# Optimization experiments

Measured on AMD Instinct MI355X. Metric: run time of the kernel, lower is better.

The kernel has to match this reference:

```python
import jax, jax.numpy as jnp
from jax import lax
import numpy as np

C = 384   # d_model (channels)
DI = 768  # d_inner = expand * C
S = 256   # d_state = min(C, 256)
R = 24    # dt_rank = ceil(C / 16)
K = 4     # d_conv
B = 2
L = 512


def setup_inputs():
    key = jax.random.key(0)
    ks = jax.random.split(key, 12)
    n = jax.random.normal
    return {
        'x': n(ks[0], (B, L, C), jnp.float32),
        'ln1_g': jnp.ones((C,), jnp.float32),
        'ln1_b': jnp.zeros((C,), jnp.float32),
        'ln2_g': jnp.ones((C,), jnp.float32),
        'ln2_b': jnp.zeros((C,), jnp.float32),
        'head_w': n(ks[1], (C, C), jnp.float32) * C ** -0.5,
        'head_b': jnp.zeros((C,), jnp.float32),
        'in_proj_w': n(ks[2], (2 * DI, C), jnp.float32) * C ** -0.5,
        'conv_w': n(ks[3], (DI, 1, K), jnp.float32) * 0.3,
        'conv_b': n(ks[4], (DI,), jnp.float32) * 0.05,
        'x_proj_w': n(ks[5], (R + 2 * S, DI), jnp.float32) * DI ** -0.5,
        'dt_proj_w': n(ks[6], (DI, R), jnp.float32) * R ** -0.5,
        'dt_proj_b': jnp.log(jnp.expm1(jax.random.uniform(ks[7], (DI,), jnp.float32, 1e-3, 0.1))),
        'A_log': jnp.log(jnp.broadcast_to(jnp.arange(1, S + 1, dtype=jnp.float32), (DI, S))),
        'D': jnp.ones((DI,), jnp.float32),
        'out_proj_w': n(ks[8], (C, DI), jnp.float32) * DI ** -0.5,
    }


def _layernorm(x, g, b, eps=1e-5):
    mu = jnp.mean(x, -1, keepdims=True)
    var = jnp.var(x, -1, keepdims=True)  # biased, as torch LayerNorm
    return (x - mu) * lax.rsqrt(var + eps) * g + b


def _mamba(u, in_proj_w, conv_w, conv_b, x_proj_w, dt_proj_w, dt_proj_b, A_log, D, out_proj_w):
    bsz = u.shape[0]
    xz = u @ in_proj_w.T                                  # (B,L,2*DI)
    x_in, z = jnp.split(xz, 2, axis=-1)
    # causal depthwise conv1d along L (left-pad K-1)
    xc = lax.conv_general_dilated(x_in.transpose(0, 2, 1), conv_w, (1,), [(K - 1, 0)],
                                  feature_group_count=DI)  # (B,DI,L)
    x_act = jax.nn.silu(xc.transpose(0, 2, 1) + conv_b)    # (B,L,DI)
    x_dbl = x_act @ x_proj_w.T                             # (B,L,R+2S)
    dt, Bm, Cm = jnp.split(x_dbl, [R, R + S], axis=-1)
    dt = jax.nn.softplus(dt @ dt_proj_w.T + dt_proj_b)     # (B,L,DI)
    A = -jnp.exp(A_log)                                    # (DI,S)
    dtu = dt * x_act                                       # (B,L,DI)

    def body(h, inp):
        dt_t, dtu_t, B_t, C_t = inp                        # (B,DI),(B,DI),(B,S),(B,S)
        dA = jnp.exp(dt_t[:, :, None] * A)                 # (B,DI,S) discretized A
        h = dA * h + dtu_t[:, :, None] * B_t[:, None, :]
        y = jnp.einsum('bds,bs->bd', h, C_t)
        return h, y

    h0 = jnp.zeros((bsz, DI, S), u.dtype)
    xs = (dt.transpose(1, 0, 2), dtu.transpose(1, 0, 2),
          Bm.transpose(1, 0, 2), Cm.transpose(1, 0, 2))
    _, ys = lax.scan(jax.checkpoint(body), h0, xs)         # ys: (L,B,DI)
    y = ys.transpose(1, 0, 2) + D * x_act                  # + D * u skip
    y = y * jax.nn.silu(z)                                 # gated output
    return y @ out_proj_w.T                                # (B,L,C)


def reference(x, ln1_g, ln1_b, ln2_g, ln2_b, head_w, head_b, in_proj_w, conv_w, conv_b,
              x_proj_w, dt_proj_w, dt_proj_b, A_log, D, out_proj_w):
    x = _mamba(_layernorm(x, ln1_g, ln1_b), in_proj_w, conv_w, conv_b, x_proj_w,
               dt_proj_w, dt_proj_b, A_log, D, out_proj_w) + x
    x = _layernorm(x, ln2_g, ln2_b) @ head_w.T + head_b + x
    return x
```

## Files before the change

### kernel.cpp

```cpp
#include <hip/hip_runtime.h>
#include <hip/hip_bf16.h>

#define Cc   384
#define DI   768
#define Ss   256
#define Rr   24
#define Kk   4
#define Bb   2
#define Ll   512
#define NROWS (Bb*Ll)
#define XZW  (2*DI)
#define XDBLW (Rr+2*Ss)
#define TC   128
#define NCH  (Ll/TC)
#define NDP  (DI/2)

#define NWA (XZW*Cc)
#define NWB (XDBLW*DI)
#define NWC (Cc*DI)
#define NWD (Cc*Cc)
#define NWTOT (NWA+NWB+NWC+NWD)
#define NWCVT_BLK (NWTOT/4/256)
#define PREP_GRID (NWCVT_BLK + NROWS/2)

typedef short v8s __attribute__((ext_vector_type(8)));
typedef float v4f __attribute__((ext_vector_type(4)));
typedef float v2f __attribute__((ext_vector_type(2)));

#if __has_builtin(__builtin_amdgcn_exp2f)
#define EXP2(x) __builtin_amdgcn_exp2f(x)
#else
#define EXP2(x) __expf((x) * 0.69314718056f)
#endif
#define L2E 1.44269504089f
#define LN2 0.69314718056f

__device__ __forceinline__ unsigned short f2bf(float f) {
    unsigned int u = __float_as_uint(f);
    unsigned int r = (u + 0x7fffu + ((u >> 16) & 1u)) >> 16;
    return (unsigned short)r;
}
__device__ __forceinline__ float bf2f(unsigned int hi) {
    return __uint_as_float(hi << 16);
}

__global__ __launch_bounds__(256) void prep_kernel(
    const float* __restrict__ wa, unsigned short* __restrict__ oa,
    const float* __restrict__ wb, unsigned short* __restrict__ ob,
    const float* __restrict__ wc, unsigned short* __restrict__ oc,
    const float* __restrict__ wd, unsigned short* __restrict__ od,
    const float* __restrict__ x, const float* __restrict__ g,
    const float* __restrict__ bia, unsigned short* __restrict__ uout)
{
    __shared__ float sm[2][4];
    if (blockIdx.x < NWCVT_BLK) {
        int i = (blockIdx.x * 256 + threadIdx.x) * 4;
        const float* src; unsigned short* dst;
        if (i < NWA)                   { src = wa + i;                     dst = oa + i; }
        else if (i < NWA + NWB)        { src = wb + (i - NWA);             dst = ob + (i - NWA); }
        else if (i < NWA + NWB + NWC)  { src = wc + (i - NWA - NWB);       dst = oc + (i - NWA - NWB); }
        else if (i < NWTOT)            { src = wd + (i - NWA - NWB - NWC); dst = od + (i - NWA - NWB - NWC); }
        else return;
        float4 v = *(const float4*)src;
        dst[0] = f2bf(v.x); dst[1] = f2bf(v.y); dst[2] = f2bf(v.z); dst[3] = f2bf(v.w);
        return;
    }
    const int half = threadIdx.x >> 7;
    const int tid  = threadIdx.x & 127;
    const int row  = (blockIdx.x - NWCVT_BLK) * 2 + half;
    const float* xr = x + (size_t)row * Cc;
    float v[3];
    float s = 0.f, q = 0.f;
#pragma unroll
    for (int i = 0; i < 3; ++i) {
        v[i] = xr[tid + i * 128];
        s += v[i];
        q += v[i] * v[i];
    }
#pragma unroll
    for (int m = 32; m; m >>= 1) {
        s += __shfl_xor(s, m);
        q += __shfl_xor(q, m);
    }
    if ((tid & 63) == 0) {
        sm[half][tid >> 6] = s;
        sm[half][2 + (tid >> 6)] = q;
    }
    __syncthreads();
    const float S_ = sm[half][0] + sm[half][1];
    const float Q_ = sm[half][2] + sm[half][3];
    const float mu = S_ * (1.f / Cc);
    const float var = Q_ * (1.f / Cc) - mu * mu;
    const float r = rsqrtf(var + 1e-5f);
#pragma unroll
    for (int i = 0; i < 3; ++i) {
        const int c = tid + i * 128;
        uout[(size_t)row * Cc + c] = f2bf((v[i] - mu) * r * g[c] + bia[c]);
    }
}

__global__ __launch_bounds__(128) void ln_bf_kernel(
    const float* __restrict__ x, const float* __restrict__ g,
    const float* __restrict__ b, unsigned short* __restrict__ out)
{
    const int row = blockIdx.x;
    const float* xr = x + (size_t)row * Cc;
    float v[3];
    float s = 0.f, q = 0.f;
#pragma unroll
    for (int i = 0; i < 3; ++i) {
        v[i] = xr[threadIdx.x + i * 128];
        s += v[i];
        q += v[i] * v[i];
    }
#pragma unroll
    for (int m = 32; m; m >>= 1) {
        s += __shfl_xor(s, m);
        q += __shfl_xor(q, m);
    }
    __shared__ float sm[4];
    if ((threadIdx.x & 63) == 0) {
        sm[threadIdx.x >> 6] = s;
        sm[2 + (threadIdx.x >> 6)] = q;
    }
    __syncthreads();
    const float S_ = sm[0] + sm[1];
    const float Q_ = sm[2] + sm[3];
    const float mu = S_ * (1.f / Cc);
    const float var = Q_ * (1.f / Cc) - mu * mu;
    const float r = rsqrtf(var + 1e-5f);
#pragma unroll
    for (int i = 0; i < 3; ++i) {
        const int c = threadIdx.x + i * 128;
        out[(size_t)row * Cc + c] = f2bf((v[i] - mu) * r * g[c] + b[c]);
    }
}

template<int EPI>
__global__ __launch_bounds__(256) void gemm_mfma(
    const unsigned short* __restrict__ A, const unsigned short* __restrict__ W,
    const float* __restrict__ bias, const float* __restrict__ res,
    float* __restrict__ out, int M, int N, int Kd)
{
    const int wave = threadIdx.x >> 6;
    const int lane = threadIdx.x & 63;
    const int m0 = blockIdx.y * 64 + (wave >> 1) * 32;
    const int n0 = blockIdx.x * 64 + (wave & 1) * 32;
    const int lr = lane & 15;
    const int quad = lane >> 4;

    v4f acc00 = {0.f,0.f,0.f,0.f}, acc01 = {0.f,0.f,0.f,0.f};
    v4f acc10 = {0.f,0.f,0.f,0.f}, acc11 = {0.f,0.f,0.f,0.f};

    int nA = n0 + lr;      if (nA >= N) nA = N - 1;
    int nB = n0 + 16 + lr; if (nB >= N) nB = N - 1;
    const unsigned short* Ar0 = A + (size_t)(m0 + lr) * Kd + quad * 8;
    const unsigned short* Ar1 = A + (size_t)(m0 + 16 + lr) * Kd + quad * 8;
    const unsigned short* Wr0 = W + (size_t)nA * Kd + quad * 8;
    const unsigned short* Wr1 = W + (size_t)nB * Kd + quad * 8;

    v8s a0 = *(const v8s*)(Ar0);
    v8s a1 = *(const v8s*)(Ar1);
    v8s b0 = *(const v8s*)(Wr0);
    v8s b1 = *(const v8s*)(Wr1);

    for (int k0 = 32; k0 < Kd; k0 += 32) {
        const v8s na0 = *(const v8s*)(Ar0 + k0);
        const v8s na1 = *(const v8s*)(Ar1 + k0);
        const v8s nb0 = *(const v8s*)(Wr0 + k0);
        const v8s nb1 = *(const v8s*)(Wr1 + k0);
        acc00 = __builtin_amdgcn_mfma_f32_16x16x32_bf16(a0, b0, acc00, 0, 0, 0);
        acc01 = __builtin_amdgcn_mfma_f32_16x16x32_bf16(a0, b1, acc01, 0, 0, 0);
        acc10 = __builtin_amdgcn_mfma_f32_16x16x32_bf16(a1, b0, acc10, 0, 0, 0);
        acc11 = __builtin_amdgcn_mfma_f32_16x16x32_bf16(a1, b1, acc11, 0, 0, 0);
        a0 = na0; a1 = na1; b0 = nb0; b1 = nb1;
    }
    acc00 = __builtin_amdgcn_mfma_f32_16x16x32_bf16(a0, b0, acc00, 0, 0, 0);
    acc01 = __builtin_amdgcn_mfma_f32_16x16x32_bf16(a0, b1, acc01, 0, 0, 0);
    acc10 = __builtin_amdgcn_mfma_f32_16x16x32_bf16(a1, b0, acc10, 0, 0, 0);
    acc11 = __builtin_amdgcn_mfma_f32_16x16x32_bf16(a1, b1, acc11, 0, 0, 0);

    v4f accs[2][2] = {{acc00, acc01}, {acc10, acc11}};
#pragma unroll
    for (int i = 0; i < 2; ++i) {
#pragma unroll
        for (int j = 0; j < 2; ++j) {
#pragma unroll
            for (int r = 0; r < 4; ++r) {
                const int row = m0 + i * 16 + quad * 4 + r;
                const int col = n0 + j * 16 + lr;
                if (col < N) {
                    float v = accs[i][j][r];
                    if (EPI >= 2) v += bias[col];
                    if (EPI >= 1) v += res[(size_t)row * N + col];
                    out[(size_t)row * N + col] = v;
                }
            }
        }
    }
}

__global__ __launch_bounds__(256) void conv_kernel(
    const float* __restrict__ xz, const float* __restrict__ cw,
    const float* __restrict__ cb, float* __restrict__ xact,
    unsigned short* __restrict__ xact_bf)
{
    const int d = blockIdx.x * 256 + threadIdx.x;
    const int l0 = blockIdx.y * 8;
    const int b  = blockIdx.z;
    const float4 w = *(const float4*)&cw[d * 4];
    const float bias = cb[d];
    float xv[11];
#pragma unroll
    for (int k = 0; k < 11; ++k) {
        const int l = l0 - 3 + k;
        xv[k] = (l >= 0 && l < Ll) ? xz[(size_t)(b * Ll + l) * XZW + d] : 0.f;
    }
#pragma unroll
    for (int i = 0; i < 8; ++i) {
        float acc = bias + w.x * xv[i] + w.y * xv[i + 1] + w.z * xv[i + 2] + w.w * xv[i + 3];
        const float sv = acc / (1.f + __expf(-acc));
        const size_t row = (size_t)(b * Ll + l0 + i);
        xact[row * DI + d] = sv;
        xact_bf[row * DI + d] = f2bf(sv);
    }
}

__global__ __launch_bounds__(NDP) void dtpack_kernel(
    const float* __restrict__ xdbl, const float* __restrict__ w,
    const float* __restrict__ bias, const float* __restrict__ xact,
    const float* __restrict__ xz, const float* __restrict__ Dp,
    float4* __restrict__ pkA, float2* __restrict__ pkB, float4* __restrict__ epk)
{
    const int dp = threadIdx.x;
    const int row0 = blockIdx.x * 4;
    __shared__ float r[4][Rr];
    if (threadIdx.x < 4 * Rr) {
        const int rr = threadIdx.x / Rr, ii = threadIdx.x % Rr;
        r[rr][ii] = xdbl[(size_t)(row0 + rr) * XDBLW + ii];
    }
    __syncthreads();
    const int d0 = dp * 2;
    float w0r[Rr], w1r[Rr];
    const float* wp = w + (size_t)d0 * Rr;
#pragma unroll
    for (int i = 0; i < Rr; ++i) { w0r[i] = wp[i]; w1r[i] = wp[Rr + i]; }
    const float b0 = bias[d0], b1 = bias[d0 + 1];
    const float D0 = Dp[d0], D1 = Dp[d0 + 1];
#pragma unroll
    for (int rr = 0; rr < 4; ++rr) {
        const int row = row0 + rr;
        float a0 = b0, a1 = b1;
#pragma unroll
        for (int i = 0; i < Rr; ++i) {
            a0 = fmaf(r[rr][i], w0r[i], a0);
            a1 = fmaf(r[rr][i], w1r[i], a1);
        }
        const float aL0 = a0 * L2E, aL1 = a1 * L2E;
        const float dtL0 = (a0 > 20.f) ? aL0 : __log2f(1.f + EXP2(aL0));
        const float dtL1 = (a1 > 20.f) ? aL1 : __log2f(1.f + EXP2(aL1));
        const float dt0 = dtL0 * LN2;
        const float dt1 = dtL1 * LN2;
        const float2 xa = *(const float2*)&xact[(size_t)row * DI + d0];
        const float2 z  = *(const float2*)&xz[(size_t)row * XZW + DI + d0];
        const float sz0 = z.x / (1.f + __expf(-z.x));
        const float sz1 = z.y / (1.f + __expf(-z.y));
        const size_t idx = (size_t)dp * NROWS + row;
        pkA[idx] = make_float4(dtL0, dt0 * xa.x, dtL1, dt1 * xa.y);
        pkB[idx] = make_float2(EXP2(-dtL0), EXP2(-dtL1));
        epk[idx] = make_float4(D0 * xa.x, sz0, D1 * xa.y, sz1);
    }
}

__global__ __launch_bounds__(64) void scan_pass1(
    const float4* __restrict__ pkA, const float2* __restrict__ pkB,
    const float* __restrict__ xdbl,
    unsigned short* __restrict__ hws, float* __restrict__ dtsum)
{
    const int lane = threadIdx.x;
    const int dp = blockIdx.x;
    const int d0 = dp * 2;
    const int c  = blockIdx.y;
    const int b  = blockIdx.z;
    const int s0 = lane * 4;
    const float s1f = (float)(s0 + 1);

    v2f h[4] = {{0.f,0.f},{0.f,0.f},{0.f,0.f},{0.f,0.f}};
    float ds0 = 0.f, ds1 = 0.f;

    const int row0 = b * Ll + c * TC;
    const size_t pk0 = (size_t)dp * NROWS + row0;
#pragma unroll 4
    for (int t = 0; t < TC; ++t) {
        const float4 P  = pkA[pk0 + t];
        const float2 Wv = pkB[pk0 + t];
        const float4 Bv = *(const float4*)&xdbl[(size_t)(row0 + t) * XDBLW + Rr + s0];
        ds0 += P.x; ds1 += P.z;
        v2f e = { EXP2(-P.x * s1f), EXP2(-P.z * s1f) };
        const v2f wv = { Wv.x, Wv.y };
        const v2f dtu = { P.y, P.w };
        h[0] = e * h[0] + dtu * Bv.x;  e *= wv;
        h[1] = e * h[1] + dtu * Bv.y;  e *= wv;
        h[2] = e * h[2] + dtu * Bv.z;  e *= wv;
        h[3] = e * h[3] + dtu * Bv.w;
    }
    const size_t base0 = (((size_t)(b * DI + d0) * NCH) + c) * Ss + s0;
    const size_t base1 = base0 + (size_t)NCH * Ss;
    uint2 o0, o1;
    o0.x = (unsigned int)f2bf(h[0].x) | ((unsigned int)f2bf(h[1].x) << 16);
    o0.y = (unsigned int)f2bf(h[2].x) | ((unsigned int)f2bf(h[3].x) << 16);
    o1.x = (unsigned int)f2bf(h[0].y) | ((unsigned int)f2bf(h[1].y) << 16);
    o1.y = (unsigned int)f2bf(h[2].y) | ((unsigned int)f2bf(h[3].y) << 16);
    *(uint2*)&hws[base0] = o0;
    *(uint2*)&hws[base1] = o1;
    if ((lane & 31) == 0) {
        const int dd = d0 + (lane >> 5);
        dtsum[(size_t)(b * DI + dd) * NCH + c] = (lane == 0) ? ds0 : ds1;
    }
}

__global__ __launch_bounds__(64) void scan_pass23(
    const float4* __restrict__ pkA, const float2* __restrict__ pkB,
    const float4* __restrict__ epk, const float* __restrict__ xdbl,
    const unsigned short* __restrict__ hws, const float* __restrict__ dtsum,
    unsigned short* __restrict__ yg_bf)
{
    __shared__ float pbuf[32][66];
    const int lane = threadIdx.x;
    const int dp = blockIdx.x;
    const int d0 = dp * 2;
    const int c  = blockIdx.y;
    const int b  = blockIdx.z;
    const int s0 = lane * 4;
    const float s1f = (float)(s0 + 1);

    const size_t base0 = (((size_t)(b * DI + d0) * NCH) + c) * Ss + s0;
    const size_t base1 = base0 + (size_t)NCH * Ss;

    v2f h[4] = {{0.f,0.f},{0.f,0.f},{0.f,0.f},{0.f,0.f}};
    {
        const float* dsr0 = dtsum + (size_t)(b * DI + d0) * NCH;
        const float* dsr1 = dsr0 + NCH;
        float Dl0 = 0.f, Dl1 = 0.f;
        for (int cp = c - 1; cp >= 0; --cp) {
            const size_t off = (size_t)(c - cp) * Ss;
            const uint2 hu0 = *(const uint2*)&hws[base0 - off];
            const uint2 hu1 = *(const uint2*)&hws[base1 - off];
            v2f e = { EXP2(-Dl0 * s1f), EXP2(-Dl1 * s1f) };
            const v2f wv = { EXP2(-Dl0), EXP2(-Dl1) };
            const v2f hl0 = { bf2f(hu0.x & 0xffffu), bf2f(hu1.x & 0xffffu) };
            const v2f hl1 = { bf2f(hu0.x >> 16),     bf2f(hu1.x >> 16) };
            const v2f hl2 = { bf2f(hu0.y & 0xffffu), bf2f(hu1.y & 0xffffu) };
            const v2f hl3 = { bf2f(hu0.y >> 16),     bf2f(hu1.y >> 16) };
            h[0] += e * hl0;  e *= wv;
            h[1] += e * hl1;  e *= wv;
            h[2] += e * hl2;  e *= wv;
            h[3] += e * hl3;
            Dl0 += dsr0[cp]; Dl1 += dsr1[cp];
        }
    }

    const int row0 = b * Ll + c * TC;
    const size_t pk0 = (size_t)dp * NROWS + row0;
    const int pidx = (lane >> 5) * 33 + (lane & 31);
    for (int seg = 0; seg < TC / 32; ++seg) {
        const int tb = seg * 32;
#pragma unroll 4
        for (int tl = 0; tl < 32; ++tl) {
            const int t = tb + tl;
            const float4 P  = pkA[pk0 + t];
            const float2 Wv = pkB[pk0 + t];
            const float4 Bv = *(const float4*)&xdbl[(size_t)(row0 + t) * XDBLW + Rr + s0];
            const float4 Cv = *(const float4*)&xdbl[(size_t)(row0 + t) * XDBLW + Rr + Ss + s0];
            v2f e = { EXP2(-P.x * s1f), EXP2(-P.z * s1f) };
            const v2f wv = { Wv.x, Wv.y };
            const v2f dtu = { P.y, P.w };
            h[0] = e * h[0] + dtu * Bv.x;  e *= wv;
            h[1] = e * h[1] + dtu * Bv.y;  e *= wv;
            h[2] = e * h[2] + dtu * Bv.z;  e *= wv;
            h[3] = e * h[3] + dtu * Bv.w;

            v2f p = h[0] * Cv.x + h[1] * Cv.y;
            p += h[2] * Cv.z + h[3] * Cv.w;
            float p0 = p.x, p1 = p.y;
            p0 += __shfl_xor(p0, 32);
            p1 += __shfl_xor(p1, 32);
            pbuf[tl][pidx] = (lane < 32) ? p0 : p1;
        }
        __syncthreads();
        {
            const int tl = lane >> 1;
            const int ch = lane & 1;
            const float* pr = &pbuf[tl][ch * 33];
            float sum = 0.f;
#pragma unroll
            for (int j = 0; j < 32; ++j) sum += pr[j];
            const float4 ev = epk[pk0 + tb + tl];
            const float Dxa = ch ? ev.z : ev.x;
            const float sz  = ch ? ev.w : ev.y;
            yg_bf[(size_t)(row0 + tb + tl) * DI + d0 + ch] = f2bf((sum + Dxa) * sz);
        }
        __syncthreads();
    }
}

extern "C" void kernel_launch(void* const* d_in, const int* in_sizes, int n_in,
                              void* d_out, int out_size, void* d_ws, size_t ws_size,
                              hipStream_t stream)
{
    const float* x         = (const float*)d_in[0];
    const float* ln1_g     = (const float*)d_in[1];
    const float* ln1_b     = (const float*)d_in[2];
    const float* ln2_g     = (const float*)d_in[3];
    const float* ln2_b     = (const float*)d_in[4];
    const float* head_w    = (const float*)d_in[5];
    const float* head_b    = (const float*)d_in[6];
    const float* in_proj_w = (const float*)d_in[7];
    const float* conv_w    = (const float*)d_in[8];
    const float* conv_b    = (const float*)d_in[9];
    const float* x_proj_w  = (const float*)d_in[10];
    const float* dt_proj_w = (const float*)d_in[11];
    const float* dt_proj_b = (const float*)d_in[12];
    const float* Dvec      = (const float*)d_in[14];
    const float* out_proj_w= (const float*)d_in[15];
    float* out = (float*)d_out;

    float* ws    = (float*)d_ws;
    float4* pkA  = (float4*)ws;
    float4* epk  = pkA + (size_t)NDP * NROWS;
    float2* pkB  = (float2*)(epk + (size_t)NDP * NROWS);
    float* xz    = (float*)(pkB + (size_t)NDP * NROWS);
    float* xact  = xz    + (size_t)NROWS * XZW;
    float* xdbl  = xact  + (size_t)NROWS * DI;
    float* x1    = xdbl  + (size_t)NROWS * XDBLW;
    float* dtsum = x1    + (size_t)NROWS * Cc;
    unsigned short* hws     = (unsigned short*)(dtsum + (size_t)Bb * DI * NCH);
    unsigned short* u_bf    = hws     + (size_t)Bb * DI * NCH * Ss;
    unsigned short* xact_bf = u_bf    + (size_t)NROWS * Cc;
    unsigned short* yg_bf   = xact_bf + (size_t)NROWS * DI;
    unsigned short* t2_bf   = yg_bf   + (size_t)NROWS * DI;
    unsigned short* ipw_bf  = t2_bf   + (size_t)NROWS * Cc;
    unsigned short* xpw_bf  = ipw_bf  + (size_t)XZW * Cc;
    unsigned short* opw_bf  = xpw_bf  + (size_t)XDBLW * DI;
    unsigned short* hw_bf   = opw_bf  + (size_t)Cc * DI;

    prep_kernel<<<PREP_GRID, 256, 0, stream>>>(
        in_proj_w, ipw_bf, x_proj_w, xpw_bf, out_proj_w, opw_bf, head_w, hw_bf,
        x, ln1_g, ln1_b, u_bf);
    gemm_mfma<0><<<dim3(24, 16), 256, 0, stream>>>(u_bf, ipw_bf, nullptr, nullptr,
                                                   xz, NROWS, XZW, Cc);
    conv_kernel<<<dim3(3, Ll / 8, Bb), 256, 0, stream>>>(xz, conv_w, conv_b,
                                                         xact, xact_bf);
    gemm_mfma<0><<<dim3(9, 16), 256, 0, stream>>>(xact_bf, xpw_bf, nullptr, nullptr,
                                                  xdbl, NROWS, XDBLW, DI);
    dtpack_kernel<<<NROWS / 4, NDP, 0, stream>>>(xdbl, dt_proj_w, dt_proj_b,
                                                 xact, xz, Dvec, pkA, pkB, epk);
    scan_pass1<<<dim3(NDP, NCH, Bb), 64, 0, stream>>>(pkA, pkB, xdbl, hws, dtsum);
    scan_pass23<<<dim3(NDP, NCH, Bb), 64, 0, stream>>>(pkA, pkB, epk, xdbl, hws,
                                                       dtsum, yg_bf);
    gemm_mfma<1><<<dim3(6, 16), 256, 0, stream>>>(yg_bf, opw_bf, nullptr, x,
                                                  x1, NROWS, Cc, DI);
    ln_bf_kernel<<<NROWS, 128, 0, stream>>>(x1, ln2_g, ln2_b, t2_bf);
    gemm_mfma<2><<<dim3(6, 16), 256, 0, stream>>>(t2_bf, hw_bf, head_b, x1,
                                                  out, NROWS, Cc, Cc);
}
```

Measured before the change: 216.1 us.

## Fold first-chunk output into scan pass one and trim redundant chunk work

Chunk 0 of the chunked selective scan needs no carried-in state, so the first scan kernel now computes its gated outputs directly, using a shared-memory reduction over the state dimension. The second kernel then only handles chunks 1..NCH-1. The first kernel also skips the last chunk, whose end state is never consumed. This removes roughly one chunk of work from each scan kernel, at the cost of load imbalance: chunk-0 blocks in the first kernel do extra C-loads, reductions and syncs.

Result: no change. 212.9 us (-1.5%).

```diff
diff --git a/kernel.cpp b/kernel.cpp
--- a/kernel.cpp
+++ b/kernel.cpp
@@ -272,11 +272,13 @@
     }
 }
 
-__global__ __launch_bounds__(64) void scan_pass1(
+__global__ __launch_bounds__(64) void scan_a(
     const float4* __restrict__ pkA, const float2* __restrict__ pkB,
-    const float* __restrict__ xdbl,
-    unsigned short* __restrict__ hws, float* __restrict__ dtsum)
-{
+    const float4* __restrict__ epk, const float* __restrict__ xdbl,
+    unsigned short* __restrict__ hws, float* __restrict__ dtsum,
+    unsigned short* __restrict__ yg_bf)
+{
+    __shared__ float pbuf[32][66];
     const int lane = threadIdx.x;
     const int dp = blockIdx.x;
     const int d0 = dp * 2;
@@ -290,20 +292,66 @@
 
     const int row0 = b * Ll + c * TC;
     const size_t pk0 = (size_t)dp * NROWS + row0;
+
+    if (c == 0) {
+        const int pidx = (lane >> 5) * 33 + (lane & 31);
+        for (int seg = 0; seg < TC / 32; ++seg) {
+            const int tb = seg * 32;
 #pragma unroll 4
-    for (int t = 0; t < TC; ++t) {
-        const float4 P  = pkA[pk0 + t];
-        const float2 Wv = pkB[pk0 + t];
-        const float4 Bv = *(const float4*)&xdbl[(size_t)(row0 + t) * XDBLW + Rr + s0];
-        ds0 += P.x; ds1 += P.z;
-        v2f e = { EXP2(-P.x * s1f), EXP2(-P.z * s1f) };
-        const v2f wv = { Wv.x, Wv.y };
-        const v2f dtu = { P.y, P.w };
-        h[0] = e * h[0] + dtu * Bv.x;  e *= wv;
-        h[1] = e * h[1] + dtu * Bv.y;  e *= wv;
-        h[2] = e * h[2] + dtu * Bv.z;  e *= wv;
-        h[3] = e * h[3] + dtu * Bv.w;
-    }
+            for (int tl = 0; tl < 32; ++tl) {
+                const int t = tb + tl;
+                const float4 P  = pkA[pk0 + t];
+                const float2 Wv = pkB[pk0 + t];
+                const float4 Bv = *(const float4*)&xdbl[(size_t)(row0 + t) * XDBLW + Rr + s0];
+                const float4 Cv = *(const float4*)&xdbl[(size_t)(row0 + t) * XDBLW + Rr + Ss + s0];
+                ds0 += P.x; ds1 += P.z;
+                v2f e = { EXP2(-P.x * s1f), EXP2(-P.z * s1f) };
+                const v2f wv = { Wv.x, Wv.y };
+                const v2f dtu = { P.y, P.w };
+                h[0] = e * h[0] + dtu * Bv.x;  e *= wv;
+                h[1] = e * h[1] + dtu * Bv.y;  e *= wv;
+                h[2] = e * h[2] + dtu * Bv.z;  e *= wv;
+                h[3] = e * h[3] + dtu * Bv.w;
+
+                v2f p = h[0] * Cv.x + h[1] * Cv.y;
+                p += h[2] * Cv.z + h[3] * Cv.w;
+                float p0 = p.x, p1 = p.y;
+                p0 += __shfl_xor(p0, 32);
+                p1 += __shfl_xor(p1, 32);
+                pbuf[tl][pidx] = (lane < 32) ? p0 : p1;
+            }
+            __syncthreads();
+            {
+                const int tl = lane >> 1;
+                const int ch = lane & 1;
+                const float* pr = &pbuf[tl][ch * 33];
+                float sum = 0.f;
+#pragma unroll
+                for (int j = 0; j < 32; ++j) sum += pr[j];
+                const float4 ev = epk[pk0 + tb + tl];
+                const float Dxa = ch ? ev.z : ev.x;
+                const float sz  = ch ? ev.w : ev.y;
+                yg_bf[(size_t)(row0 + tb + tl) * DI + d0 + ch] = f2bf((sum + Dxa) * sz);
+            }
+            __syncthreads();
+        }
+    } else {
+#pragma unroll 4
+        for (int t = 0; t < TC; ++t) {
+            const float4 P  = pkA[pk0 + t];
+            const float2 Wv = pkB[pk0 + t];
+            const float4 Bv = *(const float4*)&xdbl[(size_t)(row0 + t) * XDBLW + Rr + s0];
+            ds0 += P.x; ds1 += P.z;
+            v2f e = { EXP2(-P.x * s1f), EXP2(-P.z * s1f) };
+            const v2f wv = { Wv.x, Wv.y };
+            const v2f dtu = { P.y, P.w };
+            h[0] = e * h[0] + dtu * Bv.x;  e *= wv;
+            h[1] = e * h[1] + dtu * Bv.y;  e *= wv;
+            h[2] = e * h[2] + dtu * Bv.z;  e *= wv;
+            h[3] = e * h[3] + dtu * Bv.w;
+        }
+    }
+
     const size_t base0 = (((size_t)(b * DI + d0) * NCH) + c) * Ss + s0;
     const size_t base1 = base0 + (size_t)NCH * Ss;
     uint2 o0, o1;
@@ -319,7 +367,7 @@
     }
 }
 
-__global__ __launch_bounds__(64) void scan_pass23(
+__global__ __launch_bounds__(64) void scan_b(
     const float4* __restrict__ pkA, const float2* __restrict__ pkB,
     const float4* __restrict__ epk, const float* __restrict__ xdbl,
     const unsigned short* __restrict__ hws, const float* __restrict__ dtsum,
@@ -329,7 +377,7 @@
     const int lane = threadIdx.x;
     const int dp = blockIdx.x;
     const int d0 = dp * 2;
-    const int c  = blockIdx.y;
+    const int c  = blockIdx.y + 1;
     const int b  = blockIdx.z;
     const int s0 = lane * 4;
     const float s1f = (float)(s0 + 1);
@@ -455,9 +503,10 @@
                                                   xdbl, NROWS, XDBLW, DI);
     dtpack_kernel<<<NROWS / 4, NDP, 0, stream>>>(xdbl, dt_proj_w, dt_proj_b,
                                                  xact, xz, Dvec, pkA, pkB, epk);
-    scan_pass1<<<dim3(NDP, NCH, Bb), 64, 0, stream>>>(pkA, pkB, xdbl, hws, dtsum);
-    scan_pass23<<<dim3(NDP, NCH, Bb), 64, 0, stream>>>(pkA, pkB, epk, xdbl, hws,
-                                                       dtsum, yg_bf);
+    scan_a<<<dim3(NDP, NCH - 1, Bb), 64, 0, stream>>>(pkA, pkB, epk, xdbl,
+                                                      hws, dtsum, yg_bf);
+    scan_b<<<dim3(NDP, NCH - 1, Bb), 64, 0, stream>>>(pkA, pkB, epk, xdbl,
+                                                      hws, dtsum, yg_bf);
     gemm_mfma<1><<<dim3(6, 16), 256, 0, stream>>>(yg_bf, opw_bf, nullptr, x,
                                                   x1, NROWS, Cc, DI);
     ln_bf_kernel<<<NROWS, 128, 0, stream>>>(x1, ln2_g, ln2_b, t2_bf);
```
